# Optimization experiments

Hardware: AMD Instinct MI355X
Metric: run time of the kernel (lower is better)

## Reference

```python
import jax, jax.numpy as jnp
import numpy as np
import math

B, S, E = 16, 600, 300   # batch, seq_len, enc_len
H, NC = 512, 2           # hidden, classes
D = S * E                # archi[0] = 180000


def setup_inputs() -> dict:
    key = jax.random.key(0)
    ks = jax.random.split(key, 7)
    x = jax.random.normal(ks[0], (B, S, E), dtype=jnp.float32)
    y = jax.random.randint(ks[1], (B,), 0, NC)
    # neurons initialized to zeros (init_neurons)
    n0 = jnp.zeros((B, S, E), jnp.float32)
    n1 = jnp.zeros((B, H), jnp.float32)
    n2 = jnp.zeros((B, NC), jnp.float32)
    # Linear weights (torch layout: [out, in]), Kaiming-uniform-like scale 1/sqrt(fan_in)
    W0 = jax.random.uniform(ks[2], (E, E), jnp.float32, -1.0, 1.0) / math.sqrt(E)
    W1 = jax.random.uniform(ks[3], (H, D), jnp.float32, -1.0, 1.0) / math.sqrt(D)
    b1 = jax.random.uniform(ks[4], (H,), jnp.float32, -1.0, 1.0) / math.sqrt(D)
    W2 = jax.random.uniform(ks[5], (NC, H), jnp.float32, -1.0, 1.0) / math.sqrt(H)
    b2 = jax.random.uniform(ks[6], (NC,), jnp.float32, -1.0, 1.0) / math.sqrt(H)
    return dict(x=x, y=y, n0=n0, n1=n1, n2=n2, W0=W0, W1=W1, b1=b1, W2=W2, b2=b2, T=3)


def reference(x, y, n0, n1, n2, W0, W1, b1, W2, b2, T):
    # EqProp free-phase relaxation (beta = 0.0, forward default).
    # Analytic dPhi/dneurons replaces torch.autograd.grad:
    scale = 1.0 / math.sqrt(E)
    Wx = jnp.einsum('bse,fe->bsf', x, W0)  # synapses[0](x), constant across steps
    for _ in range(T):
        g0 = Wx + (n1 @ W1).reshape(B, S, E)              # dPhi/dn0
        g1 = n0.reshape(B, D) @ W1.T + b1 + n2 @ W2       # dPhi/dn1
        g2 = n1 @ W2.T + b2                               # dPhi/dn2 (beta=0)
        # hand-coded attention update for neuron 0: Q=g0, K=V=x
        attn = jax.nn.softmax(scale * jnp.einsum('bse,bte->bst', g0, x), axis=-1)
        n0 = jnp.einsum('bst,bte->bse', attn, x)
        n1 = jnp.tanh(g1)
        n2 = jnp.tanh(g2)
    return n0, n1, n2
```

## Files before the change

### kernel.cpp

```cpp
#include <hip/hip_runtime.h>
#include <math.h>

#define DD 180000L
#define HH 512
#define BB 16
#define SS 600
#define EE 300
#define SP 608
#define EP 320

typedef unsigned short u16;
typedef __attribute__((ext_vector_type(8))) __bf16 bf16x8;
typedef __attribute__((ext_vector_type(4))) float f32x4;

__device__ __forceinline__ u16 f2bf(float f) {
  union { float f; unsigned int u; } x; x.f = f;
  unsigned int r = (x.u + 0x7FFFu + ((x.u >> 16) & 1u)) >> 16;
  return (u16)r;
}

__global__ __launch_bounds__(256) void k_conv_x(const float* __restrict__ x,
                                                u16* __restrict__ xb, u16* __restrict__ xt) {
  __shared__ u16 tl[32][33];
  int b = blockIdx.z;
  int tt = blockIdx.x * 32, ee = blockIdx.y * 32;
  int lx = threadIdx.x & 31, ly = threadIdx.x >> 5;
#pragma unroll
  for (int i = 0; i < 4; ++i) {
    int t = tt + ly + i * 8, e = ee + lx;
    float v = (t < SS && e < EE) ? x[((long)b * SS + t) * EE + e] : 0.f;
    u16 h = f2bf(v);
    xb[((long)b * SP + t) * EP + e] = h;
    tl[ly + i * 8][lx] = h;
  }
  __syncthreads();
#pragma unroll
  for (int i = 0; i < 4; ++i) {
    int e = ee + ly + i * 8, t = tt + lx;
    xt[((long)b * EP + e) * SP + t] = tl[lx][ly + i * 8];
  }
}

__global__ __launch_bounds__(256) void k_conv_w0(const float* __restrict__ W0, u16* __restrict__ w0b) {
  int idx = blockIdx.x * 256 + threadIdx.x;
  int f = idx / EP, e = idx % EP;
  float v = (f < EE && e < EE) ? W0[f * EE + e] : 0.f;
  w0b[idx] = f2bf(v);
}

__global__ __launch_bounds__(256) void k_gemm_nt(
    const u16* __restrict__ A, int lda, long sA, int Arows,
    const u16* __restrict__ B, int ldb, long sB, int Brows,
    float* __restrict__ C, int ldc, long sC, int Mv, int Nv, int K,
    u16* __restrict__ Cb, int ldcb, long sCb) {
  int bz = blockIdx.z;
  int m0 = blockIdx.x * 64, n0 = blockIdx.y * 64;
  int lane = threadIdx.x & 63, wv = threadIdx.x >> 6;
  int wm = m0 + (wv >> 1) * 32, wn = n0 + (wv & 1) * 32;
  int q = lane >> 4, ln = lane & 15;
  const u16* Ab = A + (long)bz * sA;
  const u16* Bb = B + (long)bz * sB;
  long arow0 = (long)min(wm + ln, Arows - 1) * lda;
  long arow1 = (long)min(wm + 16 + ln, Arows - 1) * lda;
  long brow0 = (long)min(wn + ln, Brows - 1) * ldb;
  long brow1 = (long)min(wn + 16 + ln, Brows - 1) * ldb;
  f32x4 acc00 = {0.f,0.f,0.f,0.f}, acc01 = acc00, acc10 = acc00, acc11 = acc00;
  int ksteps = (K + 31) >> 5;
  for (int kk = 0; kk < ksteps; ++kk) {
    int k0 = kk * 32 + q * 8;
    bf16x8 a0 = *(const bf16x8*)(Ab + arow0 + k0);
    bf16x8 a1 = *(const bf16x8*)(Ab + arow1 + k0);
    bf16x8 b0 = *(const bf16x8*)(Bb + brow0 + k0);
    bf16x8 bv1 = *(const bf16x8*)(Bb + brow1 + k0);
    acc00 = __builtin_amdgcn_mfma_f32_16x16x32_bf16(a0, b0,  acc00, 0, 0, 0);
    acc01 = __builtin_amdgcn_mfma_f32_16x16x32_bf16(a0, bv1, acc01, 0, 0, 0);
    acc10 = __builtin_amdgcn_mfma_f32_16x16x32_bf16(a1, b0,  acc10, 0, 0, 0);
    acc11 = __builtin_amdgcn_mfma_f32_16x16x32_bf16(a1, bv1, acc11, 0, 0, 0);
  }
  float* Cp = C + (long)bz * sC;
  u16* Cbp = Cb ? (Cb + (long)bz * sCb) : (u16*)0;
#pragma unroll
  for (int sm = 0; sm < 2; ++sm) {
#pragma unroll
    for (int sn = 0; sn < 2; ++sn) {
      f32x4 acc = (sm == 0) ? ((sn == 0) ? acc00 : acc01) : ((sn == 0) ? acc10 : acc11);
#pragma unroll
      for (int r = 0; r < 4; ++r) {
        int m = wm + sm * 16 + q * 4 + r;
        int n = wn + sn * 16 + ln;
        if (m < Mv) {
          float v = acc[r];
          if (n < Nv) Cp[(long)m * ldc + n] = v;
          if (Cbp && n < ldcb) Cbp[(long)m * ldcb + n] = f2bf(n < Nv ? v : 0.f);
        }
      }
    }
  }
}

#define BN 256
#define BK 64
#define NCH 704

__global__ __launch_bounds__(256) void k_fused_w1(
    const float* __restrict__ W1, const float* __restrict__ n1f,
    const float* __restrict__ n0f, const float* __restrict__ Wx,
    u16* __restrict__ g0b, float* __restrict__ part) {
  __shared__ u16 wt[BK][BN + 8];
  __shared__ u16 n1s[BB][HH + 8];
  __shared__ u16 n0s[BB][BN + 8];
  int tid = threadIdx.x;
  long d0 = (long)blockIdx.x * BN;
#pragma unroll
  for (int i = 0; i < 8; ++i) {
    int f = i * 256 + tid;
    int b = f >> 7, c = (f & 127) * 4;
    float4 v = *(const float4*)(n1f + b * HH + c);
    n1s[b][c] = f2bf(v.x); n1s[b][c + 1] = f2bf(v.y);
    n1s[b][c + 2] = f2bf(v.z); n1s[b][c + 3] = f2bf(v.w);
  }
#pragma unroll
  for (int i = 0; i < 4; ++i) {
    int f = i * 256 + tid;
    int b = f >> 6, c = (f & 63) * 4;
    long d = d0 + c;
    float4 v = {0.f,0.f,0.f,0.f};
    if (d < DD) v = *(const float4*)(n0f + (long)b * DD + d);
    n0s[b][c] = f2bf(v.x); n0s[b][c + 1] = f2bf(v.y);
    n0s[b][c + 2] = f2bf(v.z); n0s[b][c + 3] = f2bf(v.w);
  }
  int lane = tid & 63, wv = tid >> 6, q = lane >> 4, ln = lane & 15;
  f32x4 acc0[4] = {{0.f,0.f,0.f,0.f},{0.f,0.f,0.f,0.f},{0.f,0.f,0.f,0.f},{0.f,0.f,0.f,0.f}};

  float4 pre[16];
#pragma unroll
  for (int i = 0; i < 16; ++i) {
    int f = i * 256 + tid;
    int r = f >> 6, c = (f & 63) * 4;
    long d = d0 + c;
    float4 v = {0.f,0.f,0.f,0.f};
    if (d < DD) v = *(const float4*)(W1 + (long)r * DD + d);
    pre[i] = v;
  }
  for (int s = 0; s < 8; ++s) {
    int h0 = s * BK;
    __syncthreads();
#pragma unroll
    for (int i = 0; i < 16; ++i) {
      int f = i * 256 + tid;
      int r = f >> 6, c = (f & 63) * 4;
      wt[r][c] = f2bf(pre[i].x); wt[r][c + 1] = f2bf(pre[i].y);
      wt[r][c + 2] = f2bf(pre[i].z); wt[r][c + 3] = f2bf(pre[i].w);
    }
    if (s < 7) {
#pragma unroll
      for (int i = 0; i < 16; ++i) {
        int f = i * 256 + tid;
        int r = f >> 6, c = (f & 63) * 4;
        long d = d0 + c;
        float4 v = {0.f,0.f,0.f,0.f};
        if (d < DD) v = *(const float4*)(W1 + (long)(h0 + BK + r) * DD + d);
        pre[i] = v;
      }
    }
    __syncthreads();
#pragma unroll
    for (int kst = 0; kst < 2; ++kst) {
      bf16x8 af = *(const bf16x8*)(&n1s[ln][h0 + kst * 32 + q * 8]);
#pragma unroll
      for (int nt = 0; nt < 4; ++nt) {
        int dc = wv * 64 + nt * 16 + ln;
        bf16x8 bv;
#pragma unroll
        for (int j = 0; j < 8; ++j) bv[j] = *(const __bf16*)(&wt[kst * 32 + q * 8 + j][dc]);
        acc0[nt] = __builtin_amdgcn_mfma_f32_16x16x32_bf16(af, bv, acc0[nt], 0, 0, 0);
      }
    }
    f32x4 acc1 = {0.f,0.f,0.f,0.f};
#pragma unroll
    for (int kst = 0; kst < 8; ++kst) {
      bf16x8 af = *(const bf16x8*)(&n0s[ln][kst * 32 + q * 8]);
      bf16x8 bv = *(const bf16x8*)(&wt[wv * 16 + ln][kst * 32 + q * 8]);
      acc1 = __builtin_amdgcn_mfma_f32_16x16x32_bf16(af, bv, acc1, 0, 0, 0);
    }
    long pb = (long)blockIdx.x * 8192;
#pragma unroll
    for (int r = 0; r < 4; ++r) {
      int b = q * 4 + r, h = h0 + wv * 16 + ln;
      part[pb + b * HH + h] = acc1[r];
    }
  }
#pragma unroll
  for (int nt = 0; nt < 4; ++nt) {
#pragma unroll
    for (int r = 0; r < 4; ++r) {
      int b = q * 4 + r;
      long d = d0 + wv * 64 + nt * 16 + ln;
      if (d < DD) {
        float val = Wx[(long)b * DD + d] + acc0[nt][r];
        int sI = (int)(d / EE), e = (int)(d % EE);
        g0b[((long)b * SS + sI) * EP + e] = f2bf(val);
      }
    }
  }
}

__global__ __launch_bounds__(256) void k_flash(const u16* __restrict__ g0b,
                                               const u16* __restrict__ xb,
                                               const u16* __restrict__ xt,
                                               float* __restrict__ out_n0, float scale) {
  __shared__ u16 Qs[16][328];
  __shared__ float Ss[16][609];
  __shared__ u16 Ps[16][616];
  int qt = blockIdx.x, b = blockIdx.y;
  int tid = threadIdx.x, lane = tid & 63, wv = tid >> 6, q = lane >> 4, ln = lane & 15;

#pragma unroll
  for (int i = 0; i < 3; ++i) {
    int c = tid + i * 256;
    if (c < 640) {
      int row = c / 40, cg = (c % 40) * 8;
      int qrow = min(qt * 16 + row, SS - 1);
      bf16x8 v = *(const bf16x8*)(g0b + ((long)b * SS + qrow) * EP + cg);
#pragma unroll
      for (int j = 0; j < 8; ++j) if (cg + j >= EE) v[j] = (__bf16)0.f;
      *(bf16x8*)&Qs[row][cg] = v;
    }
  }
  __syncthreads();

  f32x4 sacc[10];
#pragma unroll
  for (int i = 0; i < 10; ++i) sacc[i] = (f32x4){0.f,0.f,0.f,0.f};
  for (int k = 0; k < 10; ++k) {
    bf16x8 af = *(const bf16x8*)&Qs[ln][k * 32 + q * 8];
#pragma unroll
    for (int nt = 0; nt < 10; ++nt) {
      int tile = nt * 4 + wv;
      if (tile < 38) {
        bf16x8 bv = *(const bf16x8*)(xb + ((long)b * SP + tile * 16 + ln) * EP + k * 32 + q * 8);
        sacc[nt] = __builtin_amdgcn_mfma_f32_16x16x32_bf16(af, bv, sacc[nt], 0, 0, 0);
      }
    }
  }
#pragma unroll
  for (int nt = 0; nt < 10; ++nt) {
    int tile = nt * 4 + wv;
    if (tile < 38) {
#pragma unroll
      for (int r = 0; r < 4; ++r)
        Ss[q * 4 + r][tile * 16 + ln] = sacc[nt][r] * scale;
    }
  }
  __syncthreads();

#pragma unroll
  for (int r = 0; r < 4; ++r) {
    int row = wv * 4 + r;
    float v[10], mx = -1e30f;
#pragma unroll
    for (int i = 0; i < 10; ++i) {
      int c = lane + i * 64;
      v[i] = (c < SS) ? Ss[row][c] : -1e30f;
      mx = fmaxf(mx, v[i]);
    }
#pragma unroll
    for (int off = 1; off < 64; off <<= 1) mx = fmaxf(mx, __shfl_xor(mx, off));
    float sum = 0.f;
#pragma unroll
    for (int i = 0; i < 10; ++i) {
      int c = lane + i * 64;
      v[i] = (c < SS) ? __expf(v[i] - mx) : 0.f;
      sum += v[i];
    }
#pragma unroll
    for (int off = 1; off < 64; off <<= 1) sum += __shfl_xor(sum, off);
    float inv = 1.f / sum;
#pragma unroll
    for (int i = 0; i < 10; ++i) {
      int c = lane + i * 64;
      if (c < SP) Ps[row][c] = f2bf(v[i] * inv);
    }
  }
  __syncthreads();

  f32x4 oacc[5];
#pragma unroll
  for (int j = 0; j < 5; ++j) oacc[j] = (f32x4){0.f,0.f,0.f,0.f};
  for (int k = 0; k < 19; ++k) {
    bf16x8 af = *(const bf16x8*)&Ps[ln][k * 32 + q * 8];
#pragma unroll
    for (int j = 0; j < 5; ++j) {
      int e = (j * 4 + wv) * 16 + ln;
      bf16x8 bv = *(const bf16x8*)(xt + ((long)b * EP + e) * SP + k * 32 + q * 8);
      oacc[j] = __builtin_amdgcn_mfma_f32_16x16x32_bf16(af, bv, oacc[j], 0, 0, 0);
    }
  }
#pragma unroll
  for (int j = 0; j < 5; ++j) {
    int e = (j * 4 + wv) * 16 + ln;
    if (e < EE) {
#pragma unroll
      for (int r = 0; r < 4; ++r) {
        int qrow = qt * 16 + q * 4 + r;
        if (qrow < SS) out_n0[((long)b * SS + qrow) * EE + e] = oacc[j][r];
      }
    }
  }
}

__global__ __launch_bounds__(256) void k_init(const float* __restrict__ b1, const float* __restrict__ b2,
                                              float* __restrict__ n1, float* __restrict__ n2) {
  int idx = blockIdx.x * 256 + threadIdx.x;
  n1[idx] = tanhf(b1[idx & 511]);
  if (idx < 32) n2[idx] = tanhf(b2[idx & 1]);
}

__global__ __launch_bounds__(64) void k_g2(const float* __restrict__ n1old, const float* __restrict__ W2,
                                           const float* __restrict__ b2, float* __restrict__ n2out) {
  int b = blockIdx.x >> 1, c = blockIdx.x & 1, lane = threadIdx.x;
  float s = 0.f;
#pragma unroll
  for (int i = 0; i < 8; ++i) { int h = lane + i * 64; s += n1old[b * HH + h] * W2[c * HH + h]; }
  for (int off = 32; off; off >>= 1) s += __shfl_down(s, off);
  if (lane == 0) n2out[b * 2 + c] = tanhf(s + b2[c]);
}

__global__ __launch_bounds__(256) void k_reduce1(const float* __restrict__ part, float* __restrict__ part2) {
  int idx = blockIdx.x * 256 + threadIdx.x;
  int sl = blockIdx.y;
  float s = 0.f;
  int c0 = sl * 88;
#pragma unroll 4
  for (int c = 0; c < 88; ++c) s += part[(long)(c0 + c) * 8192 + idx];
  part2[(long)sl * 8192 + idx] = s;
}

__global__ __launch_bounds__(256) void k_reduce2(const float* __restrict__ part2, const float* __restrict__ b1,
                                                 const float* __restrict__ W2, const float* __restrict__ n2old,
                                                 float* __restrict__ n1out) {
  int idx = blockIdx.x * 256 + threadIdx.x;
  int b = idx >> 9, h = idx & 511;
  float s = b1[h] + n2old[b * 2] * W2[h] + n2old[b * 2 + 1] * W2[HH + h];
#pragma unroll
  for (int sl = 0; sl < 8; ++sl) s += part2[(long)sl * 8192 + idx];
  n1out[idx] = tanhf(s);
}

extern "C" void kernel_launch(void* const* d_in, const int* in_sizes, int n_in,
                              void* d_out, int out_size, void* d_ws, size_t ws_size,
                              hipStream_t stream) {
  const float* x  = (const float*)d_in[0];
  const float* W0 = (const float*)d_in[5];
  const float* W1 = (const float*)d_in[6];
  const float* b1 = (const float*)d_in[7];
  const float* W2 = (const float*)d_in[8];
  const float* b2 = (const float*)d_in[9];

  float* out_n0 = (float*)d_out;
  float* out_n1 = out_n0 + 16L * SS * EE;
  float* out_n2 = out_n1 + 16L * HH;

  char* w = (char*)d_ws;
  auto take = [&](size_t bytes) { char* p = w; w += (bytes + 255) & ~(size_t)255; return p; };
  u16*   xb    = (u16*)take(16L * SP * EP * 2);
  u16*   xt    = (u16*)take(16L * EP * SP * 2);
  u16*   w0b   = (u16*)take((size_t)EP * EP * 2);
  float* Wx    = (float*)take(16L * SS * EE * 4);
  u16*   g0b   = (u16*)take(16L * SS * EP * 2);
  float* part  = (float*)take((size_t)NCH * 8192 * 4);
  float* part2 = (float*)take(8L * 8192 * 4);
  float* n1A   = (float*)take(8192 * 4);
  float* n1B   = (float*)take(8192 * 4);
  float* n2A   = (float*)take(256);
  float* n2B   = (float*)take(256);

  const float scale = 1.0f / sqrtf((float)EE);

  k_conv_x<<<dim3(19, 10, 16), 256, 0, stream>>>(x, xb, xt);
  k_conv_w0<<<400, 256, 0, stream>>>(W0, w0b);
  k_gemm_nt<<<dim3(10, 5, 16), 256, 0, stream>>>(xb, EP, (long)SP * EP, SP,
                                                 w0b, EP, 0, EP,
                                                 Wx, EE, (long)SS * EE, SS, EE, EE,
                                                 g0b, EP, (long)SS * EP);
  k_init<<<32, 256, 0, stream>>>(b1, b2, n1A, n2A);

  for (int it = 0; it < 3; ++it) {
    if (it > 0) {
      const float* n1old = (it == 1) ? n1A : n1B;
      const float* n2old = (it == 1) ? n2A : n2B;
      float* n2new = (it == 1) ? n2B : out_n2;
      float* n1new = (it == 1) ? n1B : out_n1;
      k_g2<<<32, 64, 0, stream>>>(n1old, W2, b2, n2new);
      k_fused_w1<<<NCH, 256, 0, stream>>>(W1, n1old, out_n0, Wx, g0b, part);
      k_reduce1<<<dim3(32, 8), 256, 0, stream>>>(part, part2);
      k_reduce2<<<32, 256, 0, stream>>>(part2, b1, W2, n2old, n1new);
    }
    k_flash<<<dim3(38, 16), 256, 0, stream>>>(g0b, xb, xt, out_n0, scale);
  }
}
```

Before: 974.9 us.

## Merge small kernels, drop W1 register prefetch, read bf16 n1 from global

Merges W0 conversion with neuron init, and the g2, reduce1 and reduce2 kernels into one tail kernel that does a single-pass reduction over all 704 partial chunks. This cuts the launch count. k_fused_w1 drops its shared n1 tile and reads a bf16 copy of n1 from global, and removes the register prefetch of W1 so it can run 3 blocks per CU. The flash kernel hoists row pointers and fully unrolls its K loops. The tail now reduces serially over 704 chunks using only 32 blocks, and losing the W1 prefetch removes load/compute overlap.

```diff
diff --git a/kernel.cpp b/kernel.cpp
--- a/kernel.cpp
+++ b/kernel.cpp
@@ -10,6 +10,7 @@
 #define EP 320
 
 typedef unsigned short u16;
+typedef unsigned int u32;
 typedef __attribute__((ext_vector_type(8))) __bf16 bf16x8;
 typedef __attribute__((ext_vector_type(4))) float f32x4;
 
@@ -41,11 +42,24 @@
   }
 }
 
-__global__ __launch_bounds__(256) void k_conv_w0(const float* __restrict__ W0, u16* __restrict__ w0b) {
-  int idx = blockIdx.x * 256 + threadIdx.x;
-  int f = idx / EP, e = idx % EP;
-  float v = (f < EE && e < EE) ? W0[f * EE + e] : 0.f;
-  w0b[idx] = f2bf(v);
+__global__ __launch_bounds__(256) void k_cw0i(const float* __restrict__ W0, u16* __restrict__ w0b,
+                                              const float* __restrict__ b1, const float* __restrict__ b2,
+                                              float* __restrict__ n1A, u16* __restrict__ n1b,
+                                              float* __restrict__ n2A) {
+  int gb = blockIdx.x, tid = threadIdx.x;
+  if (gb < 400) {
+    int idx = gb * 256 + tid;
+    int f = idx / EP, e = idx % EP;
+    float v = (f < EE && e < EE) ? W0[f * EE + e] : 0.f;
+    w0b[idx] = f2bf(v);
+  } else {
+    int idx = (gb - 400) * 256 + tid;
+    int h = idx & 511;
+    float v = tanhf(b1[h]);
+    n1A[idx] = v;
+    n1b[idx] = f2bf(v);
+    if (idx < 32) n2A[idx] = tanhf(b2[idx & 1]);
+  }
 }
 
 __global__ __launch_bounds__(256) void k_gemm_nt(
@@ -101,24 +115,18 @@
 #define BN 256
 #define BK 64
 #define NCH 704
-
-__global__ __launch_bounds__(256) void k_fused_w1(
-    const float* __restrict__ W1, const float* __restrict__ n1f,
+#define WT_P 264
+
+__global__ __launch_bounds__(256, 3) void k_fused_w1(
+    const float* __restrict__ W1, const u16* __restrict__ n1b,
     const float* __restrict__ n0f, const float* __restrict__ Wx,
     u16* __restrict__ g0b, float* __restrict__ part) {
-  __shared__ u16 wt[BK][BN + 8];
-  __shared__ u16 n1s[BB][HH + 8];
-  __shared__ u16 n0s[BB][BN + 8];
+  __shared__ u16 wt[BK][WT_P];
+  __shared__ u16 n0s[BB][WT_P];
   int tid = threadIdx.x;
   long d0 = (long)blockIdx.x * BN;
-#pragma unroll
-  for (int i = 0; i < 8; ++i) {
-    int f = i * 256 + tid;
-    int b = f >> 7, c = (f & 127) * 4;
-    float4 v = *(const float4*)(n1f + b * HH + c);
-    n1s[b][c] = f2bf(v.x); n1s[b][c + 1] = f2bf(v.y);
-    n1s[b][c + 2] = f2bf(v.z); n1s[b][c + 3] = f2bf(v.w);
-  }
+  int lane = tid & 63, wv = tid >> 6, q = lane >> 4, ln = lane & 15;
+
 #pragma unroll
   for (int i = 0; i < 4; ++i) {
     int f = i * 256 + tid;
@@ -129,19 +137,8 @@
     n0s[b][c] = f2bf(v.x); n0s[b][c + 1] = f2bf(v.y);
     n0s[b][c + 2] = f2bf(v.z); n0s[b][c + 3] = f2bf(v.w);
   }
-  int lane = tid & 63, wv = tid >> 6, q = lane >> 4, ln = lane & 15;
+
   f32x4 acc0[4] = {{0.f,0.f,0.f,0.f},{0.f,0.f,0.f,0.f},{0.f,0.f,0.f,0.f},{0.f,0.f,0.f,0.f}};
-
-  float4 pre[16];
-#pragma unroll
-  for (int i = 0; i < 16; ++i) {
-    int f = i * 256 + tid;
-    int r = f >> 6, c = (f & 63) * 4;
-    long d = d0 + c;
-    float4 v = {0.f,0.f,0.f,0.f};
-    if (d < DD) v = *(const float4*)(W1 + (long)r * DD + d);
-    pre[i] = v;
-  }
   for (int s = 0; s < 8; ++s) {
     int h0 = s * BK;
     __syncthreads();
@@ -149,24 +146,16 @@
     for (int i = 0; i < 16; ++i) {
       int f = i * 256 + tid;
       int r = f >> 6, c = (f & 63) * 4;
-      wt[r][c] = f2bf(pre[i].x); wt[r][c + 1] = f2bf(pre[i].y);
-      wt[r][c + 2] = f2bf(pre[i].z); wt[r][c + 3] = f2bf(pre[i].w);
-    }
-    if (s < 7) {
-#pragma unroll
-      for (int i = 0; i < 16; ++i) {
-        int f = i * 256 + tid;
-        int r = f >> 6, c = (f & 63) * 4;
-        long d = d0 + c;
-        float4 v = {0.f,0.f,0.f,0.f};
-        if (d < DD) v = *(const float4*)(W1 + (long)(h0 + BK + r) * DD + d);
-        pre[i] = v;
-      }
+      long d = d0 + c;
+      float4 v = {0.f,0.f,0.f,0.f};
+      if (d < DD) v = *(const float4*)(W1 + (long)(h0 + r) * DD + d);
+      wt[r][c] = f2bf(v.x); wt[r][c + 1] = f2bf(v.y);
+      wt[r][c + 2] = f2bf(v.z); wt[r][c + 3] = f2bf(v.w);
     }
     __syncthreads();
 #pragma unroll
     for (int kst = 0; kst < 2; ++kst) {
-      bf16x8 af = *(const bf16x8*)(&n1s[ln][h0 + kst * 32 + q * 8]);
+      bf16x8 af = *(const bf16x8*)(n1b + ln * HH + h0 + kst * 32 + q * 8);
 #pragma unroll
       for (int nt = 0; nt < 4; ++nt) {
         int dc = wv * 64 + nt * 16 + ln;
@@ -179,16 +168,14 @@
     f32x4 acc1 = {0.f,0.f,0.f,0.f};
 #pragma unroll
     for (int kst = 0; kst < 8; ++kst) {
-      bf16x8 af = *(const bf16x8*)(&n0s[ln][kst * 32 + q * 8]);
-      bf16x8 bv = *(const bf16x8*)(&wt[wv * 16 + ln][kst * 32 + q * 8]);
+      bf16x8 af = *(const bf16x8*)&n0s[ln][kst * 32 + q * 8];
+      bf16x8 bv = *(const bf16x8*)&wt[wv * 16 + ln][kst * 32 + q * 8];
       acc1 = __builtin_amdgcn_mfma_f32_16x16x32_bf16(af, bv, acc1, 0, 0, 0);
     }
     long pb = (long)blockIdx.x * 8192;
 #pragma unroll
-    for (int r = 0; r < 4; ++r) {
-      int b = q * 4 + r, h = h0 + wv * 16 + ln;
-      part[pb + b * HH + h] = acc1[r];
-    }
+    for (int r = 0; r < 4; ++r)
+      part[pb + (q * 4 + r) * HH + h0 + wv * 16 + ln] = acc1[r];
   }
 #pragma unroll
   for (int nt = 0; nt < 4; ++nt) {
@@ -229,16 +216,22 @@
   }
   __syncthreads();
 
+  const u16* xrow[10];
+#pragma unroll
+  for (int nt = 0; nt < 10; ++nt) {
+    int tile = nt * 4 + wv;
+    xrow[nt] = xb + ((long)b * SP + min(tile, 37) * 16 + ln) * EP;
+  }
   f32x4 sacc[10];
 #pragma unroll
   for (int i = 0; i < 10; ++i) sacc[i] = (f32x4){0.f,0.f,0.f,0.f};
+#pragma unroll
   for (int k = 0; k < 10; ++k) {
     bf16x8 af = *(const bf16x8*)&Qs[ln][k * 32 + q * 8];
 #pragma unroll
     for (int nt = 0; nt < 10; ++nt) {
-      int tile = nt * 4 + wv;
-      if (tile < 38) {
-        bf16x8 bv = *(const bf16x8*)(xb + ((long)b * SP + tile * 16 + ln) * EP + k * 32 + q * 8);
+      if (nt * 4 + wv < 38) {
+        bf16x8 bv = *(const bf16x8*)(xrow[nt] + k * 32 + q * 8);
         sacc[nt] = __builtin_amdgcn_mfma_f32_16x16x32_bf16(af, bv, sacc[nt], 0, 0, 0);
       }
     }
@@ -284,15 +277,21 @@
   }
   __syncthreads();
 
+  const u16* xtrow[5];
+#pragma unroll
+  for (int j = 0; j < 5; ++j) {
+    int e = (j * 4 + wv) * 16 + ln;
+    xtrow[j] = xt + ((long)b * EP + e) * SP;
+  }
   f32x4 oacc[5];
 #pragma unroll
   for (int j = 0; j < 5; ++j) oacc[j] = (f32x4){0.f,0.f,0.f,0.f};
+#pragma unroll
   for (int k = 0; k < 19; ++k) {
     bf16x8 af = *(const bf16x8*)&Ps[ln][k * 32 + q * 8];
 #pragma unroll
     for (int j = 0; j < 5; ++j) {
-      int e = (j * 4 + wv) * 16 + ln;
-      bf16x8 bv = *(const bf16x8*)(xt + ((long)b * EP + e) * SP + k * 32 + q * 8);
+      bf16x8 bv = *(const bf16x8*)(xtrow[j] + k * 32 + q * 8);
       oacc[j] = __builtin_amdgcn_mfma_f32_16x16x32_bf16(af, bv, oacc[j], 0, 0, 0);
     }
   }
@@ -309,42 +308,27 @@
   }
 }
 
-__global__ __launch_bounds__(256) void k_init(const float* __restrict__ b1, const float* __restrict__ b2,
-                                              float* __restrict__ n1, float* __restrict__ n2) {
-  int idx = blockIdx.x * 256 + threadIdx.x;
-  n1[idx] = tanhf(b1[idx & 511]);
-  if (idx < 32) n2[idx] = tanhf(b2[idx & 1]);
-}
-
-__global__ __launch_bounds__(64) void k_g2(const float* __restrict__ n1old, const float* __restrict__ W2,
-                                           const float* __restrict__ b2, float* __restrict__ n2out) {
-  int b = blockIdx.x >> 1, c = blockIdx.x & 1, lane = threadIdx.x;
-  float s = 0.f;
-#pragma unroll
-  for (int i = 0; i < 8; ++i) { int h = lane + i * 64; s += n1old[b * HH + h] * W2[c * HH + h]; }
-  for (int off = 32; off; off >>= 1) s += __shfl_down(s, off);
-  if (lane == 0) n2out[b * 2 + c] = tanhf(s + b2[c]);
-}
-
-__global__ __launch_bounds__(256) void k_reduce1(const float* __restrict__ part, float* __restrict__ part2) {
-  int idx = blockIdx.x * 256 + threadIdx.x;
-  int sl = blockIdx.y;
-  float s = 0.f;
-  int c0 = sl * 88;
-#pragma unroll 4
-  for (int c = 0; c < 88; ++c) s += part[(long)(c0 + c) * 8192 + idx];
-  part2[(long)sl * 8192 + idx] = s;
-}
-
-__global__ __launch_bounds__(256) void k_reduce2(const float* __restrict__ part2, const float* __restrict__ b1,
-                                                 const float* __restrict__ W2, const float* __restrict__ n2old,
-                                                 float* __restrict__ n1out) {
-  int idx = blockIdx.x * 256 + threadIdx.x;
-  int b = idx >> 9, h = idx & 511;
-  float s = b1[h] + n2old[b * 2] * W2[h] + n2old[b * 2 + 1] * W2[HH + h];
-#pragma unroll
-  for (int sl = 0; sl < 8; ++sl) s += part2[(long)sl * 8192 + idx];
-  n1out[idx] = tanhf(s);
+__global__ __launch_bounds__(256) void k_tail2(
+    const float* __restrict__ part, const float* __restrict__ b1,
+    const float* __restrict__ W2, const float* __restrict__ b2,
+    const float* __restrict__ n1old, const float* __restrict__ n2old,
+    float* __restrict__ n1new, u16* __restrict__ n1bnew, float* __restrict__ n2new) {
+  if (blockIdx.x < 32) {
+    int idx = blockIdx.x * 256 + threadIdx.x;
+    int b = idx >> 9, h = idx & 511;
+    float s = b1[h] + n2old[b * 2] * W2[h] + n2old[b * 2 + 1] * W2[HH + h];
+    const float* p = part + idx;
+#pragma unroll 8
+    for (int c = 0; c < NCH; ++c) s += p[(long)c * 8192];
+    float v = tanhf(s);
+    n1new[idx] = v;
+    n1bnew[idx] = f2bf(v);
+  } else if (threadIdx.x < 32) {
+    int b = threadIdx.x >> 1, c = threadIdx.x & 1;
+    float s = 0.f;
+    for (int h = 0; h < HH; ++h) s += n1old[b * HH + h] * W2[c * HH + h];
+    n2new[b * 2 + c] = tanhf(s + b2[c]);
+  }
 }
 
 extern "C" void kernel_launch(void* const* d_in, const int* in_sizes, int n_in,
@@ -369,7 +353,7 @@
   float* Wx    = (float*)take(16L * SS * EE * 4);
   u16*   g0b   = (u16*)take(16L * SS * EP * 2);
   float* part  = (float*)take((size_t)NCH * 8192 * 4);
-  float* part2 = (float*)take(8L * 8192 * 4);
+  u16*   n1b   = (u16*)take(8192 * 2);
   float* n1A   = (float*)take(8192 * 4);
   float* n1B   = (float*)take(8192 * 4);
   float* n2A   = (float*)take(256);
@@ -378,23 +362,21 @@
   const float scale = 1.0f / sqrtf((float)EE);
 
   k_conv_x<<<dim3(19, 10, 16), 256, 0, stream>>>(x, xb, xt);
-  k_conv_w0<<<400, 256, 0, stream>>>(W0, w0b);
+  k_cw0i<<<432, 256, 0, stream>>>(W0, w0b, b1, b2, n1A, n1b, n2A);
   k_gemm_nt<<<dim3(10, 5, 16), 256, 0, stream>>>(xb, EP, (long)SP * EP, SP,
                                                  w0b, EP, 0, EP,
                                                  Wx, EE, (long)SS * EE, SS, EE, EE,
                                                  g0b, EP, (long)SS * EP);
-  k_init<<<32, 256, 0, stream>>>(b1, b2, n1A, n2A);
 
   for (int it = 0; it < 3; ++it) {
     if (it > 0) {
       const float* n1old = (it == 1) ? n1A : n1B;
       const float* n2old = (it == 1) ? n2A : n2B;
+      float* n1new = (it == 1) ? n1B : out_n1;
       float* n2new = (it == 1) ? n2B : out_n2;
-      float* n1new = (it == 1) ? n1B : out_n1;
-      k_g2<<<32, 64, 0, stream>>>(n1old, W2, b2, n2new);
-      k_fused_w1<<<NCH, 256, 0, stream>>>(W1, n1old, out_n0, Wx, g0b, part);
-      k_reduce1<<<dim3(32, 8), 256, 0, stream>>>(part, part2);
-      k_reduce2<<<32, 256, 0, stream>>>(part2, b1, W2, n2old, n1new);
+      k_fused_w1<<<NCH, 256, 0, stream>>>(W1, n1b, out_n0, Wx, g0b, part);
+      k_tail2<<<33, 256, 0, stream>>>(part, b1, W2, b2, n1old, n2old,
+                                      n1new, n1b, n2new);
     }
     k_flash<<<dim3(38, 16), 256, 0, stream>>>(g0b, xb, xt, out_n0, scale);
   }
```

New measurement: 1.025 ms. 1.05x slower.
